# Performance work log

Measured on AMD Instinct MI355X. Metric: run time of the kernel, lower is better.

The kernel has to match this reference:

```python
import jax, jax.numpy as jnp
import numpy as np

DEPTH = 2
DIM = 1024     # shot-embedding width
SDIM = 256     # SSM state width
B = 256        # batch (episodes x classes)
S = 64         # shots per class (scan length)
EPS = 1e-5


def setup_inputs() -> dict:
    key = jax.random.key(0)
    ks = jax.random.split(key, 10)
    sc = 0.02
    return {
        "shot_embeddings": jax.random.normal(ks[0], (B, S, DIM), jnp.float32),
        # per-layer selective-scan cell params (stacked over depth)
        "Wd": jax.random.normal(ks[1], (DEPTH, DIM, SDIM), jnp.float32) * sc,   # delta proj
        "bd": jnp.zeros((DEPTH, SDIM), jnp.float32),
        "Wi": jax.random.normal(ks[2], (DEPTH, DIM, SDIM), jnp.float32) * sc,   # input (B) proj
        "bi": jnp.zeros((DEPTH, SDIM), jnp.float32),
        "A_log": jax.random.normal(ks[3], (DEPTH, SDIM), jnp.float32),          # state decay param
        "Wo": jax.random.normal(ks[4], (DEPTH, SDIM, DIM), jnp.float32) * sc,   # readout (C) proj
        "bo": jnp.zeros((DEPTH, DIM), jnp.float32),
        # state_to_class Linear(state_dim, dim) per layer
        "Ws": jax.random.normal(ks[5], (DEPTH, SDIM, DIM), jnp.float32) * sc,
        "bs": jnp.zeros((DEPTH, DIM), jnp.float32),
        # LayerNorm
        "gamma": jnp.ones((DIM,), jnp.float32),
        "beta": jnp.zeros((DIM,), jnp.float32),
    }


def _run_selective_scan(x, Wd, bd, Wi, bi, A_log, Wo, bo):
    """Mamba-style selective scan over the shot axis.
    x: [B,S,D] -> (y: [B,S,D], final_state: [B,N])"""
    delta = jax.nn.softplus(jnp.einsum('bsd,dn->bsn', x, Wd) + bd)   # [B,S,N]
    u = jnp.einsum('bsd,dn->bsn', x, Wi) + bi                        # [B,S,N]
    decay = jnp.exp(-delta * jax.nn.softplus(A_log))                 # [B,S,N]
    drive = delta * u                                                # [B,S,N]

    def step(h, t):
        d, g = t
        h = d * h + g
        return h, h

    h0 = jnp.zeros((x.shape[0], Wd.shape[1]), x.dtype)
    final, hs = jax.lax.scan(step, h0, (decay.swapaxes(0, 1), drive.swapaxes(0, 1)))
    hs = hs.swapaxes(0, 1)                                           # [B,S,N]
    y = jnp.einsum('bsn,nd->bsd', hs, Wo) + bo                       # [B,S,D]
    return y, final


def reference(shot_embeddings, Wd, bd, Wi, bi, A_log, Wo, bo, Ws, bs, gamma, beta):
    hidden = shot_embeddings
    class_state = None
    for l in range(Wd.shape[0]):  # fixed small depth
        hidden, state = _run_selective_scan(hidden, Wd[l], bd[l], Wi[l], bi[l],
                                            A_log[l], Wo[l], bo[l])
        class_state = jnp.einsum('bn,nd->bd', state, Ws[l]) + bs[l]   # [B,D]
        hidden = hidden + class_state[:, None, :]
    pooled = class_state + hidden.mean(axis=1)                        # [B,D]
    mu = pooled.mean(axis=-1, keepdims=True)
    var = pooled.var(axis=-1, keepdims=True)
    class_repr = (pooled - mu) / jnp.sqrt(var + EPS) * gamma + beta
    return class_repr, hidden
```

## Files before the change

### kernel.cpp

```cpp
#include <hip/hip_runtime.h>
#include <hip/hip_bf16.h>

#define DEPTH 2
#define DIM   1024
#define SDIM  256
#define BATCH 256
#define SHOTS 64
#define M_TOT (BATCH*SHOTS)
#define SGRP  4
#define GSTEP (SHOTS/SGRP)

typedef __attribute__((ext_vector_type(8))) short bf16x8;
typedef __attribute__((ext_vector_type(4))) float f32x4;
typedef unsigned short u16;

__device__ __forceinline__ u16 f2bf(float f) {
    union { float f; unsigned u; } v; v.f = f;
    unsigned r = v.u + 0x7fffu + ((v.u >> 16) & 1u);
    return (u16)(r >> 16);
}

__device__ __forceinline__ unsigned pk_bf2(float a, float b) {
    union { __hip_bfloat162 h2; unsigned u; } c;
    c.h2 = __float22bfloat162_rn(make_float2(a, b));
    return c.u;
}

__device__ __forceinline__ float bf2f(u16 h) {
    union { unsigned u; float f; } c; c.u = (unsigned)h << 16; return c.f;
}

__device__ __forceinline__ float softplus_f(float x) {
    if (x > 20.f) return x;
    return log1pf(__expf(x));
}

__device__ __forceinline__ void gld16(const u16* g, u16* l) {
    __builtin_amdgcn_global_load_lds(
        (const __attribute__((address_space(1))) unsigned int*)g,
        (__attribute__((address_space(3))) unsigned int*)l, 16, 0, 0);
}

__device__ __forceinline__ void transpose_body(
    float T[64][65], const float* __restrict__ A1, const float* __restrict__ A2,
    u16* __restrict__ out, int K, int N, int SPLIT, int k0, int n0, int layer,
    int tid)
{
    const bool first = (n0 < SPLIT);
    const int scols = first ? SPLIT : (N - SPLIT);
    const float* S = (first ? A1 : A2) + (size_t)layer * K * scols
                     + (first ? n0 : (n0 - SPLIT));
    out += (size_t)layer * K * N;

    #pragma unroll
    for (int i = 0; i < 4; ++i) {
        const int c = tid + i * 256;
        const int kr = c >> 4, cc = c & 15;
        const float4 v = *(const float4*)(S + (size_t)(k0 + kr) * scols + cc * 4);
        T[kr][cc * 4 + 0] = v.x; T[kr][cc * 4 + 1] = v.y;
        T[kr][cc * 4 + 2] = v.z; T[kr][cc * 4 + 3] = v.w;
    }
    __syncthreads();
    #pragma unroll
    for (int i = 0; i < 4; ++i) {
        const int c = tid + i * 256;
        const int nr = c >> 4, cc = c & 15;
        ushort4 h;
        h.x = f2bf(T[cc * 4 + 0][nr]); h.y = f2bf(T[cc * 4 + 1][nr]);
        h.z = f2bf(T[cc * 4 + 2][nr]); h.w = f2bf(T[cc * 4 + 3][nr]);
        *(ushort4*)&out[(size_t)(n0 + nr) * K + k0 + cc * 4] = h;
    }
}

__global__ __launch_bounds__(256)
void prep(const float* __restrict__ Wd, const float* __restrict__ Wi,
          const float* __restrict__ Wo, const float* __restrict__ Ws,
          const float* __restrict__ X0,
          u16* __restrict__ WcombT, u16* __restrict__ WoT,
          u16* __restrict__ Wsb, u16* __restrict__ Xbf)
{
    __shared__ float T[64][65];
    const int bid = blockIdx.x;
    const int tid = threadIdx.x;

    if (bid < 256) {
        const int kx = bid & 15, ny = (bid >> 4) & 7, lz = bid >> 7;
        transpose_body(T, Wd, Wi, WcombT, 1024, 512, 256, kx * 64, ny * 64, lz, tid);
    } else if (bid < 384) {
        const int sub = bid - 256;
        const int kx = sub & 3, ny = (sub >> 2) & 15, lz = sub >> 6;
        transpose_body(T, Wo, Wo, WoT, 256, 1024, 1024, kx * 64, ny * 64, lz, tid);
    } else if (bid < 640) {
        const size_t i = ((size_t)(bid - 384) * 256 + tid) * 8;
        const float4 a = *(const float4*)(Ws + i);
        const float4 b = *(const float4*)(Ws + i + 4);
        int4 o;
        o.x = (int)pk_bf2(a.x, a.y); o.y = (int)pk_bf2(a.z, a.w);
        o.z = (int)pk_bf2(b.x, b.y); o.w = (int)pk_bf2(b.z, b.w);
        *(int4*)(Wsb + i) = o;
    } else {
        const size_t total = (size_t)M_TOT * DIM;
        const size_t stride = (size_t)2048 * 256 * 8;
        for (size_t i = ((size_t)(bid - 640) * 256 + tid) * 8; i < total; i += stride) {
            const float4 a = *(const float4*)(X0 + i);
            const float4 b = *(const float4*)(X0 + i + 4);
            int4 o;
            o.x = (int)pk_bf2(a.x, a.y); o.y = (int)pk_bf2(a.z, a.w);
            o.z = (int)pk_bf2(b.x, b.y); o.w = (int)pk_bf2(b.z, b.w);
            *(int4*)(Xbf + i) = o;
        }
    }
}

#define BM 128
#define BN 128
#define BK 32

template<int EPI, bool SWIZ, bool BF16OUT, bool POOL>
__global__ __launch_bounds__(256)
void gemm_bf16(const u16* __restrict__ A, const u16* __restrict__ BT,
               void* __restrict__ Cv, const float* __restrict__ bo,
               const float* __restrict__ cs, float* __restrict__ pooled,
               int K, int ldc, int CB)
{
    __shared__ __align__(16) u16 As[BM * BK];
    __shared__ __align__(16) u16 Bs[BN * BK];

    const int tid = threadIdx.x;
    const int id  = blockIdx.x;
    int rb, cb;
    if (SWIZ) {
        const int xcd = id & 7, slot = id >> 3;
        rb = xcd + 8 * (slot / CB);
        cb = slot % CB;
    } else {
        rb = id / CB; cb = id % CB;
    }
    const int row0 = rb * BM, col0 = cb * BN;

    const int l  = tid & 63;
    const int w  = tid >> 6;
    const int wm = (w >> 1) * 64, wn = (w & 1) * 64;
    const int lr = l & 15, lq = l >> 4;

    const int sg   = w * 2;
    const int srow = l >> 2;
    const int scol = (l & 3) * 8;
    const u16* Ag = A  + (size_t)(row0 + sg * 16 + srow) * K + scol;
    const u16* Bg = BT + (size_t)(col0 + sg * 16 + srow) * K + scol;
    u16* Asd = &As[sg * 512 + l * 8];
    u16* Bsd = &Bs[sg * 512 + l * 8];

    f32x4 acc[4][4];
    #pragma unroll
    for (int i = 0; i < 4; ++i)
        #pragma unroll
        for (int j = 0; j < 4; ++j)
            acc[i][j] = (f32x4){0.f, 0.f, 0.f, 0.f};

    for (int k0 = 0; k0 < K; k0 += BK) {
        gld16(Ag + k0,                  Asd);
        gld16(Ag + (size_t)16 * K + k0, Asd + 512);
        gld16(Bg + k0,                  Bsd);
        gld16(Bg + (size_t)16 * K + k0, Bsd + 512);
        __syncthreads();

        bf16x8 af[4], bfr[4];
        #pragma unroll
        for (int i = 0; i < 4; ++i)
            af[i] = *(const bf16x8*)&As[(wm + i * 16 + lr) * BK + lq * 8];
        #pragma unroll
        for (int j = 0; j < 4; ++j)
            bfr[j] = *(const bf16x8*)&Bs[(wn + j * 16 + lr) * BK + lq * 8];

        #pragma unroll
        for (int i = 0; i < 4; ++i)
            #pragma unroll
            for (int j = 0; j < 4; ++j)
                acc[i][j] = __builtin_amdgcn_mfma_f32_16x16x32_bf16(
                    af[i], bfr[j], acc[i][j], 0, 0, 0);
        __syncthreads();
    }

    float psum[4] = {0.f, 0.f, 0.f, 0.f};
    #pragma unroll
    for (int i = 0; i < 4; ++i) {
        const int grow = row0 + wm + i * 16 + lq * 4;
        #pragma unroll
        for (int j = 0; j < 4; ++j) {
            const int gcol = col0 + wn + j * 16 + lr;
            float addv = 0.f;
            if (EPI >= 1) addv += bo[gcol];
            if (EPI == 2) addv += cs[(size_t)(grow >> 6) * DIM + gcol];
            #pragma unroll
            for (int r = 0; r < 4; ++r) {
                const float val = acc[i][j][r] + addv;
                if (BF16OUT) ((u16*)Cv)[(size_t)(grow + r) * ldc + gcol] = f2bf(val);
                else         ((float*)Cv)[(size_t)(grow + r) * ldc + gcol] = val;
                if (POOL) psum[j] += val;
            }
        }
    }
    if (POOL) {
        const int batch_w = (row0 + wm) >> 6;
        #pragma unroll
        for (int j = 0; j < 4; ++j) {
            float v = psum[j];
            v += __shfl_xor(v, 16, 64);
            v += __shfl_xor(v, 32, 64);
            if (lq == 0)
                pooled[(size_t)batch_w * DIM + col0 + wn + j * 16 + lr] = v;
        }
    }
}

__global__ __launch_bounds__(1024)
void scan_cs(const float* __restrict__ PQ,
             const float* __restrict__ bd, const float* __restrict__ bi,
             const float* __restrict__ A_log,
             const u16* __restrict__ Wsb, const float* __restrict__ bs,
             u16* __restrict__ hsb, float* __restrict__ csbuf)
{
    const int b = blockIdx.x;
    const int n = threadIdx.x & 255;
    const int g = threadIdx.x >> 8;
    const float bdv = bd[n], biv = bi[n];
    const float spA = softplus_f(A_log[n]);
    const size_t m0 = (size_t)b * SHOTS + g * GSTEP;
    const float* base = PQ + m0 * 512 + n;

    float dec[GSTEP], drv[GSTEP];
    #pragma unroll
    for (int s = 0; s < GSTEP; ++s) {
        dec[s] = base[s * 512];
        drv[s] = base[s * 512 + SDIM];
    }
    float a = 1.f, hl = 0.f;
    #pragma unroll
    for (int s = 0; s < GSTEP; ++s) {
        const float delta = softplus_f(dec[s] + bdv);
        const float d  = __expf(-delta * spA);
        const float gv = delta * (drv[s] + biv);
        dec[s] = d; drv[s] = gv;
        a *= d; hl = d * hl + gv;
    }

    __shared__ float2 grp[SGRP][SDIM];
    __shared__ float st[SDIM];
    grp[g][n] = make_float2(a, hl);
    __syncthreads();

    float h = 0.f;
    for (int j = 0; j < g; ++j) {
        const float2 sv = grp[j][n];
        h = sv.x * h + sv.y;
    }

    u16* hout = hsb + m0 * SDIM + n;
    #pragma unroll
    for (int s = 0; s < GSTEP; ++s) {
        h = dec[s] * h + drv[s];
        hout[s * SDIM] = f2bf(h);
    }
    if (g == SGRP - 1) st[n] = h;
    __syncthreads();

    const int d = threadIdx.x;
    float c = bs[d];
    const u16* wp = Wsb + d;
    #pragma unroll 8
    for (int k = 0; k < SDIM; ++k)
        c += st[k] * bf2f(wp[(size_t)k * DIM]);
    csbuf[(size_t)b * DIM + d] = c;
}

__global__ __launch_bounds__(1024)
void final_kernel(const float* __restrict__ pooled, const float* __restrict__ cs,
                  const float* __restrict__ gamma, const float* __restrict__ beta,
                  float* __restrict__ out)
{
    const int b = blockIdx.x;
    const int d = threadIdx.x;

    const float p = cs[(size_t)b * DIM + d]
                  + pooled[(size_t)b * DIM + d] * (1.f / SHOTS);

    __shared__ float rsum[1024], rsq[1024];
    rsum[d] = p; rsq[d] = p * p;
    __syncthreads();
    for (int off = 512; off > 0; off >>= 1) {
        if (d < off) { rsum[d] += rsum[d + off]; rsq[d] += rsq[d + off]; }
        __syncthreads();
    }
    const float mu  = rsum[0] * (1.f / DIM);
    const float var = rsq[0] * (1.f / DIM) - mu * mu;
    const float inv = rsqrtf(var + 1e-5f);

    out[(size_t)b * DIM + d] = (p - mu) * inv * gamma[d] + beta[d];
}


extern "C" void kernel_launch(void* const* d_in, const int* in_sizes, int n_in,
                              void* d_out, int out_size, void* d_ws, size_t ws_size,
                              hipStream_t stream)
{
    const float* X0    = (const float*)d_in[0];
    const float* Wd    = (const float*)d_in[1];
    const float* bd    = (const float*)d_in[2];
    const float* Wi    = (const float*)d_in[3];
    const float* bi    = (const float*)d_in[4];
    const float* A_log = (const float*)d_in[5];
    const float* Wo    = (const float*)d_in[6];
    const float* bo    = (const float*)d_in[7];
    const float* Ws    = (const float*)d_in[8];
    const float* bs    = (const float*)d_in[9];
    const float* gamma = (const float*)d_in[10];
    const float* beta  = (const float*)d_in[11];

    float* out_cr     = (float*)d_out;
    float* out_hidden = out_cr + (size_t)BATCH * DIM;

    u16* Xbf = (u16*)out_hidden;

    char* w = (char*)d_ws;
    float*  PQ     = (float*)w;  w += (size_t)M_TOT * 512 * 4;
    float*  csbuf  = (float*)w;  w += (size_t)BATCH * DIM * 4;
    float*  pooled = (float*)w;  w += (size_t)BATCH * DIM * 4;
    u16*    hsb    = (u16*)w;    w += (size_t)M_TOT * SDIM * 2;
    u16*    WcombT = (u16*)w;    w += (size_t)DEPTH * 512 * 1024 * 2;
    u16*    WoT    = (u16*)w;    w += (size_t)DEPTH * 1024 * 256 * 2;
    u16*    Wsb    = (u16*)w;    w += (size_t)DEPTH * SDIM * DIM * 2;

    prep<<<2688, 256, 0, stream>>>(Wd, Wi, Wo, Ws, X0, WcombT, WoT, Wsb, Xbf);

    for (int l = 0; l < DEPTH; ++l) {
        gemm_bf16<0, true, false, false><<<512, 256, 0, stream>>>(
            Xbf, WcombT + (size_t)l * 512 * 1024, PQ, nullptr, nullptr, nullptr,
            1024, 512, 4);
        scan_cs<<<BATCH, 1024, 0, stream>>>(
            PQ, bd + l * SDIM, bi + l * SDIM, A_log + l * SDIM,
            Wsb + (size_t)l * SDIM * DIM, bs + l * DIM, hsb, csbuf);
        if (l < DEPTH - 1) {
            gemm_bf16<2, true, true, false><<<1024, 256, 0, stream>>>(
                hsb, WoT + (size_t)l * 1024 * 256, Xbf, bo + l * DIM, csbuf,
                nullptr, 256, 1024, 8);
        } else {
            gemm_bf16<2, true, false, true><<<1024, 256, 0, stream>>>(
                hsb, WoT + (size_t)l * 1024 * 256, out_hidden, bo + l * DIM, csbuf,
                pooled, 256, 1024, 8);
        }
    }
    final_kernel<<<BATCH, 1024, 0, stream>>>(pooled, csbuf, gamma, beta, out_cr);
}
```

Before: 296.5 us.

## Stage scan coefficients in LDS and split-K the state-to-class matvec

The scan kernel now keeps per-step decay and drive values in shared memory instead of register arrays, which lowers register pressure in the 1024-thread block. The state_to_class matvec is reorganised so each thread computes four output columns over a quarter of K with vectorised bf16 loads, followed by an LDS reduction across the four groups. Softplus switches to the fast __logf form with a lower cutoff. In exchange the kernel uses much more LDS and adds a barrier, and softplus precision drops slightly.

```diff
diff --git a/kernel.cpp b/kernel.cpp
--- a/kernel.cpp
+++ b/kernel.cpp
@@ -31,8 +31,8 @@
 }
 
 __device__ __forceinline__ float softplus_f(float x) {
-    if (x > 20.f) return x;
-    return log1pf(__expf(x));
+    if (x > 15.f) return x;
+    return __logf(1.f + __expf(x));
 }
 
 __device__ __forceinline__ void gld16(const u16* g, u16* l) {
@@ -221,32 +221,32 @@
              const u16* __restrict__ Wsb, const float* __restrict__ bs,
              u16* __restrict__ hsb, float* __restrict__ csbuf)
 {
+    __shared__ __align__(16) float decS[GSTEP][1024];
+    __shared__ float drvS[GSTEP][1024];
+    __shared__ float2 grp[SGRP][SDIM];
+    __shared__ float st[SDIM];
+
+    const int tid = threadIdx.x;
     const int b = blockIdx.x;
-    const int n = threadIdx.x & 255;
-    const int g = threadIdx.x >> 8;
+    const int n = tid & 255;
+    const int g = tid >> 8;
     const float bdv = bd[n], biv = bi[n];
     const float spA = softplus_f(A_log[n]);
     const size_t m0 = (size_t)b * SHOTS + g * GSTEP;
     const float* base = PQ + m0 * 512 + n;
 
-    float dec[GSTEP], drv[GSTEP];
+    float a = 1.f, hl = 0.f;
     #pragma unroll
     for (int s = 0; s < GSTEP; ++s) {
-        dec[s] = base[s * 512];
-        drv[s] = base[s * 512 + SDIM];
-    }
-    float a = 1.f, hl = 0.f;
-    #pragma unroll
-    for (int s = 0; s < GSTEP; ++s) {
-        const float delta = softplus_f(dec[s] + bdv);
+        const float p = base[s * 512];
+        const float q = base[s * 512 + SDIM];
+        const float delta = softplus_f(p + bdv);
         const float d  = __expf(-delta * spA);
-        const float gv = delta * (drv[s] + biv);
-        dec[s] = d; drv[s] = gv;
+        const float gv = delta * (q + biv);
+        decS[s][tid] = d; drvS[s][tid] = gv;
         a *= d; hl = d * hl + gv;
     }
 
-    __shared__ float2 grp[SGRP][SDIM];
-    __shared__ float st[SDIM];
     grp[g][n] = make_float2(a, hl);
     __syncthreads();
 
@@ -259,19 +259,36 @@
     u16* hout = hsb + m0 * SDIM + n;
     #pragma unroll
     for (int s = 0; s < GSTEP; ++s) {
-        h = dec[s] * h + drv[s];
+        h = decS[s][tid] * h + drvS[s][tid];
         hout[s * SDIM] = f2bf(h);
     }
     if (g == SGRP - 1) st[n] = h;
     __syncthreads();
 
-    const int d = threadIdx.x;
-    float c = bs[d];
-    const u16* wp = Wsb + d;
+    const int dbase = n * 4;
+    f32x4 part = {0.f, 0.f, 0.f, 0.f};
+    const int kq = g * 64;
     #pragma unroll 8
-    for (int k = 0; k < SDIM; ++k)
-        c += st[k] * bf2f(wp[(size_t)k * DIM]);
-    csbuf[(size_t)b * DIM + d] = c;
+    for (int k = 0; k < 64; ++k) {
+        const float sk = st[kq + k];
+        const ushort4 wv = *(const ushort4*)&Wsb[(size_t)(kq + k) * DIM + dbase];
+        part[0] += sk * bf2f(wv.x); part[1] += sk * bf2f(wv.y);
+        part[2] += sk * bf2f(wv.z); part[3] += sk * bf2f(wv.w);
+    }
+    f32x4* psum = (f32x4*)decS;
+    psum[g * 256 + n] = part;
+    __syncthreads();
+    if (tid < 256) {
+        const f32x4 s0 = psum[tid], s1 = psum[256 + tid];
+        const f32x4 s2 = psum[512 + tid], s3 = psum[768 + tid];
+        const float4 bv = *(const float4*)(bs + tid * 4);
+        float4 o;
+        o.x = bv.x + s0[0] + s1[0] + s2[0] + s3[0];
+        o.y = bv.y + s0[1] + s1[1] + s2[1] + s3[1];
+        o.z = bv.z + s0[2] + s1[2] + s2[2] + s3[2];
+        o.w = bv.w + s0[3] + s1[3] + s2[3] + s3[3];
+        *(float4*)(csbuf + (size_t)b * DIM + tid * 4) = o;
+    }
 }
 
 __global__ __launch_bounds__(1024)
```

Measured after the change: 272.3 us. 8.1% less time.
